# Kernel optimization log

Hardware: AMD Instinct MI355X
Metric: run time of the kernel (lower is better)

The kernel has to match this reference:

```python
import jax, jax.numpy as jnp
import numpy as np

C = 1.0      # base manifold curvature (Lorentz c)
C_E = 1.0    # expert manifold curvature (all experts init to c=1.0)
K = 1        # n_activated_experts (top-k)
SCALE = 2.0  # LResNet scale for shared-expert combine
EPS = 1e-8


def _lorentz_swiglu(x, W1, W3, W2, c_mid, c_out, prescale):
    """LorentzExpert / LorentzFeedForward: SwiGLU on space coords with Lorentz time lift.
    x: [T, D] (full Lorentz vector). W1,W3: [I-1, D]; W2: [D-1, I]. Returns [T, D]."""
    if prescale:
        x = x * np.float32(np.sqrt(C_E / C))  # x * sqrt(c_expert / c)
    s1 = jax.nn.silu(x @ W1.T)                 # [T, I-1] w1(x, return_space=True)
    s3 = x @ W3.T                              # [T, I-1] w3(x, return_space=True)
    sp = s1 * s3                               # gated space part
    t = jnp.sqrt(jnp.clip((sp * sp).sum(-1, keepdims=True) + c_mid, EPS))
    h = jnp.concatenate([t, sp], axis=-1)      # [T, I] point on expert manifold
    o = h @ W2.T                               # [T, D-1] w2 space output
    ot = jnp.sqrt(jnp.clip((o * o).sum(-1, keepdims=True) + c_out, EPS))
    return jnp.concatenate([ot, o], axis=-1)   # [T, D] on base manifold


def setup_inputs() -> dict:
    key = jax.random.key(0)
    ks = jax.random.split(key, 9)
    T, D, E, I = 2048, 1024, 8, 1024
    x = jax.random.normal(ks[0], (T, D), jnp.float32)
    gate_w = jax.random.normal(ks[1], (E, D - 1), jnp.float32) / np.sqrt(D - 1)
    gate_b = jax.random.normal(ks[2], (E,), jnp.float32) * 0.01
    W1 = jax.random.normal(ks[3], (E, I - 1, D), jnp.float32) / np.sqrt(D)
    W3 = jax.random.normal(ks[4], (E, I - 1, D), jnp.float32) / np.sqrt(D)
    W2 = jax.random.normal(ks[5], (E, D - 1, I), jnp.float32) / np.sqrt(I)
    Ws1 = jax.random.normal(ks[6], (I - 1, D), jnp.float32) / np.sqrt(D)
    Ws3 = jax.random.normal(ks[7], (I - 1, D), jnp.float32) / np.sqrt(D)
    Ws2 = jax.random.normal(ks[8], (D - 1, I), jnp.float32) / np.sqrt(I)
    return {"x": x, "gate_w": gate_w, "gate_b": gate_b, "W1": W1, "W3": W3,
            "W2": W2, "Ws1": Ws1, "Ws3": Ws3, "Ws2": Ws2}


def reference(x, gate_w, gate_b, W1, W3, W2, Ws1, Ws3, Ws2):
    T, D = x.shape
    E = gate_w.shape[0]
    # ---- Gate (softmax scoring, n_groups == 1, route_scale == 1.0) ----
    logits = x[:, 1:] @ gate_w.T                                    # [T, E]
    scores = jax.nn.softmax(logits.astype(jnp.float32), axis=-1)
    biased = scores + gate_b                                        # bias only affects routing
    _, idx = jax.lax.top_k(biased, K)                               # [T, K]
    weights = jnp.take_along_axis(scores, idx, axis=-1).astype(x.dtype)  # [T, K]
    # dense per-token expert gate weights [T, E]
    oh = jax.nn.one_hot(idx, E, dtype=x.dtype)                      # [T, K, E]
    gw = (oh * weights[..., None]).sum(axis=1)                      # [T, E]
    # ---- y init: project(zeros) -> [sqrt(c), 0, ..., 0] ----
    y0 = jnp.concatenate([jnp.full((T, 1), np.sqrt(C), x.dtype),
                          jnp.zeros((T, D - 1), x.dtype)], axis=-1)
    # ---- routed experts (dense reference: every expert on every token, masked combine) ----
    e_out = jax.vmap(lambda w1, w3, w2: _lorentz_swiglu(x, w1, w3, w2, C_E, C, True))(W1, W3, W2)  # [E, T, D]
    y = y0 + jnp.einsum('te,etd->td', gw, e_out)
    # ---- shared expert (LorentzFeedForward, stays on base manifold) ----
    z = _lorentz_swiglu(x, Ws1, Ws3, Ws2, C, C, False)
    # ---- LResNet weighted sum: normalize (z + scale*y) back to manifold ----
    comb = z + SCALE * y
    li = (comb[:, 1:] ** 2).sum(-1, keepdims=True) - comb[:, :1] ** 2  # Lorentz inner <comb,comb>
    out = np.float32(np.sqrt(C)) * comb / jnp.sqrt(jnp.clip(jnp.abs(li), EPS))
    return out
```

## Files before the change

### kernel.cpp

```cpp
#include <hip/hip_runtime.h>

typedef __bf16 bf16;
typedef __attribute__((ext_vector_type(8))) __bf16 bf16x8;
typedef __attribute__((ext_vector_type(4))) float floatx4;

#define TOK 2048
#define DD  1024
#define NE  8
#define SMAX 24

#define MFMA16(A,B,C) __builtin_amdgcn_mfma_f32_16x16x32_bf16(A,B,C,0,0,0)

__device__ __forceinline__ void load_lds16(const bf16* g, bf16* l) {
  __builtin_amdgcn_global_load_lds(
      (const __attribute__((address_space(1))) void*)g,
      (__attribute__((address_space(3))) void*)l, 16, 0, 0);
}

#define WBAR(N) asm volatile("s_waitcnt vmcnt(" #N ")\n\ts_barrier" ::: "memory")
#define BARO    asm volatile("s_barrier" ::: "memory")

#define NCVT (8*2046 + 2046 + 8*1023 + 1023)
#define GATEB TOK
#define ZEROB TOK
__global__ __launch_bounds__(256) void prep_kernel(
    const float* __restrict__ x, const float* __restrict__ gate_w,
    const float* __restrict__ gate_b,
    const float* __restrict__ W1, const float* __restrict__ W3,
    const float* __restrict__ W2, const float* __restrict__ Ws1,
    const float* __restrict__ Ws3, const float* __restrict__ Ws2,
    bf16* __restrict__ x_bf, int* __restrict__ eidx, float* __restrict__ ewgt,
    float* __restrict__ ss,
    bf16* __restrict__ w13, bf16* __restrict__ ws13,
    bf16* __restrict__ w2b, bf16* __restrict__ ws2b,
    float* __restrict__ o_r, float* __restrict__ o_s)
{
  const int bid = blockIdx.x, tid = threadIdx.x;

  if (bid >= GATEB) {
    if (bid >= GATEB + NCVT) {
      const int t = bid - (GATEB + NCVT);
      const float4 z = {0.f, 0.f, 0.f, 0.f};
      ((float4*)(o_r + (size_t)t * 1024))[tid] = z;
      ((float4*)(o_s + (size_t)t * 1024))[tid] = z;
      return;
    }
    const int r = bid - GATEB;
    const float* src; bf16* dst;
    if (r < 8 * 2046) {
      const int e = r / 2046, q = r % 2046;
      src = ((q & 1) ? W3 : W1) + ((size_t)e * 1023 + (q >> 1)) * 1024;
      dst = w13 + (size_t)r * 1024;
    } else if (r < 8 * 2046 + 2046) {
      const int q = r - 8 * 2046;
      src = ((q & 1) ? Ws3 : Ws1) + (size_t)(q >> 1) * 1024;
      dst = ws13 + (size_t)q * 1024;
    } else if (r < 8 * 2046 + 2046 + 8 * 1023) {
      const int q = r - (8 * 2046 + 2046);
      src = W2 + (size_t)q * 1024;
      dst = w2b + (size_t)q * 1024;
    } else {
      const int q = r - (8 * 2046 + 2046 + 8 * 1023);
      src = Ws2 + (size_t)q * 1024;
      dst = ws2b + (size_t)q * 1024;
    }
    const float4 f = ((const float4*)src)[tid];
    union { bf16 h[4]; uint2 u; } p;
    p.h[0] = (bf16)f.x; p.h[1] = (bf16)f.y; p.h[2] = (bf16)f.z; p.h[3] = (bf16)f.w;
    ((uint2*)dst)[tid] = p.u;
    return;
  }

  const int t = bid;
  if (tid < 2) ss[tid * TOK + t] = 0.f;
  const float4 v = ((const float4*)(x + (size_t)t * DD))[tid];
  union { bf16 h[4]; uint2 u; } pk;
  pk.h[0] = (bf16)v.x; pk.h[1] = (bf16)v.y; pk.h[2] = (bf16)v.z; pk.h[3] = (bf16)v.w;
  ((uint2*)(x_bf + (size_t)t * DD))[tid] = pk.u;

  float acc[NE];
#pragma unroll
  for (int e = 0; e < NE; ++e) acc[e] = 0.f;
  const float vv[4] = {v.x, v.y, v.z, v.w};
#pragma unroll
  for (int i = 0; i < 4; ++i) {
    const int d = tid * 4 + i;
    if (d >= 1) {
#pragma unroll
      for (int e = 0; e < NE; ++e) acc[e] += vv[i] * gate_w[e * (DD - 1) + d - 1];
    }
  }
#pragma unroll
  for (int off = 32; off > 0; off >>= 1) {
#pragma unroll
    for (int e = 0; e < NE; ++e) acc[e] += __shfl_down(acc[e], off);
  }
  __shared__ float red[4][NE];
  const int wid = tid >> 6, lane = tid & 63;
  if (lane == 0) {
#pragma unroll
    for (int e = 0; e < NE; ++e) red[wid][e] = acc[e];
  }
  __syncthreads();
  if (tid == 0) {
    float lg[NE];
#pragma unroll
    for (int e = 0; e < NE; ++e) lg[e] = red[0][e] + red[1][e] + red[2][e] + red[3][e];
    float m = lg[0];
    for (int e = 1; e < NE; ++e) m = fmaxf(m, lg[e]);
    float ex[NE], s = 0.f;
    for (int e = 0; e < NE; ++e) { ex[e] = expf(lg[e] - m); s += ex[e]; }
    const float inv = 1.f / s;
    int best = 0; float bb = ex[0] * inv + gate_b[0];
    for (int e = 1; e < NE; ++e) {
      const float b = ex[e] * inv + gate_b[e];
      if (b > bb) { bb = b; best = e; }
    }
    eidx[t] = best;
    ewgt[t] = ex[best] * inv;
  }
}

__global__ __launch_bounds__(256) void route_kernel(
    const int* __restrict__ eidx, int* __restrict__ perm,
    int* __restrict__ pos_of, int4* __restrict__ wl, int* __restrict__ n1)
{
  __shared__ int cnt[NE], off[NE], bas[NE + 1];
  const int tid = threadIdx.x;
  if (tid < NE) cnt[tid] = 0;
  __syncthreads();
  for (int t = tid; t < TOK; t += 256) atomicAdd(&cnt[eidx[t]], 1);
  __syncthreads();
  if (tid == 0) {
    int run = 0;
    for (int e = 0; e < NE; ++e) { bas[e] = run; off[e] = run; run += cnt[e]; }
    bas[NE] = run;
    int n = 0;
    for (int e = 0; e < NE; ++e)
      for (int r0 = 0; r0 < cnt[e]; r0 += 256) {
        int rows = cnt[e] - r0; if (rows > 256) rows = 256;
        wl[n++] = make_int4(bas[e] + r0, rows, e, 0);
      }
    for (int r0 = 0; r0 < TOK; r0 += 256) wl[n++] = make_int4(r0, 256, NE, 0);
    *n1 = n;
  }
  __syncthreads();
  for (int t = tid; t < TOK; t += 256) {
    const int e = eidx[t];
    const int p = atomicAdd(&off[e], 1);
    perm[p] = t;
    pos_of[t] = p;
  }
}

__global__ __launch_bounds__(1024) void mlp1_kernel(
    const bf16* __restrict__ x_bf, const bf16* __restrict__ w13,
    const bf16* __restrict__ ws13,
    const int* __restrict__ perm, const int4* __restrict__ wl,
    const int* __restrict__ wl_n,
    bf16* __restrict__ h_r, bf16* __restrict__ h_s,
    float* __restrict__ ss_r, float* __restrict__ ss_z)
{
  const int bid = blockIdx.x;
  const int slot = bid % SMAX, nt = bid / SMAX;
  if (slot >= *wl_n) return;
  const int4 wle = wl[slot];
  const int mbase = wle.x, rows = wle.y, eid = wle.z;
  const int tid = threadIdx.x;
  const bool routed = (eid < NE);
  const bf16* bmat = routed ? w13 + (size_t)eid * 2046 * 1024 : ws13;
  bf16* hbuf  = routed ? h_r : h_s;
  float* ssbuf = routed ? ss_r : ss_z;

  extern __shared__ __align__(16) bf16 smem[];
  bf16* const Asb[2] = {smem, smem + 16384};
  bf16* const Bsb[2] = {smem + 32768, smem + 49152};
  __shared__ int toks[256];
  if (tid < 256) {
    int r = tid < rows ? tid : rows - 1;
    toks[tid] = routed ? perm[mbase + r] : (mbase + r);
  }
  __syncthreads();

  const int wid = tid >> 6, lane = tid & 63;
  const int srow = lane >> 3;
  const int kbg  = (lane & 7) ^ (srow & 7);
  const bf16 *aG0, *aG1, *bG0, *bG1;
  int aL0o, aL1o, bL0o, bL1o;
  {
    const int r0 = wid * 16;
    aG0 = x_bf + (size_t)toks[r0 + 0 + srow] * 1024 + kbg * 8;
    aG1 = x_bf + (size_t)toks[r0 + 8 + srow] * 1024 + kbg * 8;
    aL0o = (r0 + 0) * 64; aL1o = (r0 + 8) * 64;
    int b0 = nt * 256 + r0 + 0 + srow; if (b0 > 2045) b0 = 2045;
    int b1 = nt * 256 + r0 + 8 + srow; if (b1 > 2045) b1 = 2045;
    bG0 = bmat + (size_t)b0 * 1024 + kbg * 8;
    bG1 = bmat + (size_t)b1 * 1024 + kbg * 8;
    bL0o = (r0 + 0) * 64; bL1o = (r0 + 8) * 64;
  }

  const int lrow = lane & 15, quad = lane >> 4, sw = lane & 7;
  const int wrow = (wid >> 2) * 64, wcol = (wid & 3) * 64;
  int aoff[4], boff[4], koff[2];
#pragma unroll
  for (int mi = 0; mi < 4; ++mi) aoff[mi] = (wrow + mi * 16 + lrow) * 64;
#pragma unroll
  for (int ni = 0; ni < 4; ++ni) boff[ni] = (wcol + ni * 16 + lrow) * 64;
#pragma unroll
  for (int kk = 0; kk < 2; ++kk) koff[kk] = ((kk * 4 + quad) ^ sw) * 8;

  const floatx4 fz = {0.f, 0.f, 0.f, 0.f};
  floatx4 acc[4][4];
#pragma unroll
  for (int mi = 0; mi < 4; ++mi)
#pragma unroll
    for (int ni = 0; ni < 4; ++ni) acc[mi][ni] = fz;

#define STAGE1(KE, BUF) { \
    load_lds16(aG0 + (KE), Asb[BUF] + aL0o); load_lds16(aG1 + (KE), Asb[BUF] + aL1o); \
    load_lds16(bG0 + (KE), Bsb[BUF] + bL0o); load_lds16(bG1 + (KE), Bsb[BUF] + bL1o); }

#define COMP1(BUF) { \
_Pragma("unroll") \
    for (int kk = 0; kk < 2; ++kk) { \
      bf16x8 av[4], bv[4]; \
_Pragma("unroll") \
      for (int mi = 0; mi < 4; ++mi) av[mi] = *(const bf16x8*)(Asb[BUF] + aoff[mi] + koff[kk]); \
_Pragma("unroll") \
      for (int ni = 0; ni < 4; ++ni) bv[ni] = *(const bf16x8*)(Bsb[BUF] + boff[ni] + koff[kk]); \
_Pragma("unroll") \
      for (int mi = 0; mi < 4; ++mi) \
_Pragma("unroll") \
        for (int ni = 0; ni < 4; ++ni) \
          acc[mi][ni] = MFMA16(av[mi], bv[ni], acc[mi][ni]); \
    } }

  STAGE1(0, 0)
  STAGE1(64, 1)
#pragma unroll 1
  for (int t = 0; t < 7; ++t) {
    const int ke = t * 128;
    WBAR(4); COMP1(0) BARO; STAGE1(ke + 128, 0)
    WBAR(4); COMP1(1) BARO; STAGE1(ke + 192, 1)
  }
  WBAR(4); COMP1(0)
  WBAR(0); COMP1(1)
#undef STAGE1
#undef COMP1

#pragma unroll
  for (int mi = 0; mi < 4; ++mi) {
#pragma unroll
    for (int r = 0; r < 4; ++r) {
      const int row = wrow + mi * 16 + quad * 4 + r;
      const bool rowok = row < rows;
      float ssum = 0.f;
#pragma unroll
      for (int ni = 0; ni < 4; ++ni) {
        const float c = acc[mi][ni][r];
        const float partner = __shfl_xor(c, 1);
        const float s1 = (lane & 1) ? partner : c;
        const float s3 = (lane & 1) ? c : partner;
        const float sp = (s1 / (1.f + __expf(-s1))) * s3;
        const int P = (nt * 256 + wcol + ni * 16 + lrow) >> 1;
        const bool ok = rowok && ((lane & 1) == 0) && (P < 1023);
        if (ok) hbuf[(size_t)(mbase + row) * 1024 + 1 + P] = (bf16)sp;
        ssum += ok ? sp * sp : 0.f;
      }
      ssum += __shfl_xor(ssum, 1);
      ssum += __shfl_xor(ssum, 2);
      ssum += __shfl_xor(ssum, 4);
      ssum += __shfl_xor(ssum, 8);
      if (lrow == 0 && rowok) atomicAdd(ssbuf + mbase + row, ssum);
    }
  }
}

__global__ __launch_bounds__(256) void finalize_t_kernel(
    const float* __restrict__ ss_r, const float* __restrict__ ss_z,
    bf16* __restrict__ h_r, bf16* __restrict__ h_s)
{
  const int i = blockIdx.x * 256 + threadIdx.x;
  if (i < TOK) {
    h_r[(size_t)i * 1024] = (bf16)sqrtf(ss_r[i] + 1.0f);
    h_s[(size_t)i * 1024] = (bf16)sqrtf(ss_z[i] + 1.0f);
  }
}

__global__ __launch_bounds__(1024) void mlp2_kernel(
    const bf16* __restrict__ h_r, const bf16* __restrict__ h_s,
    const bf16* __restrict__ w2b, const bf16* __restrict__ ws2b,
    const int4* __restrict__ wl, const int* __restrict__ wl_n,
    float* __restrict__ o_r, float* __restrict__ o_s)
{
  const int bid = blockIdx.x;
  const int slot = bid % SMAX;
  const int rest = bid / SMAX;
  const int nt = rest & 3, kh = rest >> 2;
  if (slot >= *wl_n) return;
  const int4 wle = wl[slot];
  const int mbase = wle.x, rows = wle.y, eid = wle.z;
  const int tid = threadIdx.x;
  const bool routed = (eid < NE);
  const bf16* abuf = routed ? h_r : h_s;
  const bf16* bmat = routed ? w2b + (size_t)eid * 1023 * 1024 : ws2b;
  float* obuf = routed ? o_r : o_s;
  const int n0 = nt * 256;
  const int kbase = kh * 512;

  extern __shared__ __align__(16) bf16 smem[];
  bf16* const Asb[2] = {smem, smem + 16384};
  bf16* const Bsb[2] = {smem + 32768, smem + 49152};

  const int wid = tid >> 6, lane = tid & 63;
  const int srow = lane >> 3;
  const int kbg  = (lane & 7) ^ (srow & 7);
  const bf16 *aG0, *aG1, *bG0, *bG1;
  int aL0o, aL1o, bL0o, bL1o;
  {
    const int r0 = wid * 16;
    int ra0 = r0 + 0 + srow; if (ra0 >= rows) ra0 = rows - 1;
    int ra1 = r0 + 8 + srow; if (ra1 >= rows) ra1 = rows - 1;
    aG0 = abuf + (size_t)(mbase + ra0) * 1024 + kbase + kbg * 8;
    aG1 = abuf + (size_t)(mbase + ra1) * 1024 + kbase + kbg * 8;
    aL0o = (r0 + 0) * 64; aL1o = (r0 + 8) * 64;
    int b0 = n0 + r0 + 0 + srow; if (b0 > 1022) b0 = 1022;
    int b1 = n0 + r0 + 8 + srow; if (b1 > 1022) b1 = 1022;
    bG0 = bmat + (size_t)b0 * 1024 + kbase + kbg * 8;
    bG1 = bmat + (size_t)b1 * 1024 + kbase + kbg * 8;
    bL0o = (r0 + 0) * 64; bL1o = (r0 + 8) * 64;
  }

  const int lrow = lane & 15, quad = lane >> 4, sw = lane & 7;
  const int wrow = (wid >> 2) * 64, wcol = (wid & 3) * 64;
  int aoff[4], boff[4], koff[2];
#pragma unroll
  for (int mi = 0; mi < 4; ++mi) aoff[mi] = (wrow + mi * 16 + lrow) * 64;
#pragma unroll
  for (int ni = 0; ni < 4; ++ni) boff[ni] = (wcol + ni * 16 + lrow) * 64;
#pragma unroll
  for (int kk = 0; kk < 2; ++kk) koff[kk] = ((kk * 4 + quad) ^ sw) * 8;

  const floatx4 fz = {0.f, 0.f, 0.f, 0.f};
  floatx4 acc[4][4];
#pragma unroll
  for (int mi = 0; mi < 4; ++mi)
#pragma unroll
    for (int ni = 0; ni < 4; ++ni) acc[mi][ni] = fz;

#define STAGE2(KE, BUF) { \
    load_lds16(aG0 + (KE), Asb[BUF] + aL0o); load_lds16(aG1 + (KE), Asb[BUF] + aL1o); \
    load_lds16(bG0 + (KE), Bsb[BUF] + bL0o); load_lds16(bG1 + (KE), Bsb[BUF] + bL1o); }

#define COMP2(BUF) { \
_Pragma("unroll") \
    for (int kk = 0; kk < 2; ++kk) { \
      bf16x8 av[4], bv[4]; \
_Pragma("unroll") \
      for (int mi = 0; mi < 4; ++mi) av[mi] = *(const bf16x8*)(Asb[BUF] + aoff[mi] + koff[kk]); \
_Pragma("unroll") \
      for (int ni = 0; ni < 4; ++ni) bv[ni] = *(const bf16x8*)(Bsb[BUF] + boff[ni] + koff[kk]); \
_Pragma("unroll") \
      for (int mi = 0; mi < 4; ++mi) \
_Pragma("unroll") \
        for (int ni = 0; ni < 4; ++ni) \
          acc[mi][ni] = MFMA16(av[mi], bv[ni], acc[mi][ni]); \
    } }

  STAGE2(0, 0)
  STAGE2(64, 1)
#pragma unroll 1
  for (int t = 0; t < 3; ++t) {
    const int ke = t * 128;
    WBAR(4); COMP2(0) BARO; STAGE2(ke + 128, 0)
    WBAR(4); COMP2(1) BARO; STAGE2(ke + 192, 1)
  }
  WBAR(4); COMP2(0)
  WBAR(0); COMP2(1)
#undef STAGE2
#undef COMP2

#pragma unroll
  for (int mi = 0; mi < 4; ++mi) {
#pragma unroll
    for (int r = 0; r < 4; ++r) {
      const int row = wrow + mi * 16 + quad * 4 + r;
      if (row < rows) {
        float* orow = obuf + (size_t)(mbase + row) * 1024;
#pragma unroll
        for (int ni = 0; ni < 4; ++ni) {
          const int n = n0 + wcol + ni * 16 + lrow;
          if (n < 1023) atomicAdd(orow + n, acc[mi][ni][r]);
        }
      }
    }
  }
}

__global__ __launch_bounds__(256) void combine_kernel(
    const float* __restrict__ o_r, const float* __restrict__ o_s,
    const int* __restrict__ pos_of, const float* __restrict__ wgt,
    float* __restrict__ out)
{
  const int t = blockIdx.x, tid = threadIdx.x;
  const int p = pos_of[t];
  const float w = wgt[t];
  const float4 oz = ((const float4*)(o_s + (size_t)t * 1024))[tid];
  const float4 oe = ((const float4*)(o_r + (size_t)p * 1024))[tid];
  const float tw = 2.f * w;
  float c0 = oz.x + tw * oe.x;
  float c1 = oz.y + tw * oe.y;
  float c2 = oz.z + tw * oe.z;
  float c3 = (tid == 255) ? 0.f : (oz.w + tw * oe.w);
  float sc = c0 * c0 + c1 * c1 + c2 * c2 + c3 * c3;
  float sz = oz.x * oz.x + oz.y * oz.y + oz.z * oz.z + ((tid == 255) ? 0.f : oz.w * oz.w);
  float sr = oe.x * oe.x + oe.y * oe.y + oe.z * oe.z + ((tid == 255) ? 0.f : oe.w * oe.w);
#pragma unroll
  for (int off = 32; off > 0; off >>= 1) {
    sc += __shfl_down(sc, off);
    sz += __shfl_down(sz, off);
    sr += __shfl_down(sr, off);
  }
  __shared__ float rs[3][4];
  if ((tid & 63) == 0) {
    rs[0][tid >> 6] = sc; rs[1][tid >> 6] = sz; rs[2][tid >> 6] = sr;
  }
  __syncthreads();
  const float space2 = rs[0][0] + rs[0][1] + rs[0][2] + rs[0][3];
  const float ss_oz  = rs[1][0] + rs[1][1] + rs[1][2] + rs[1][3];
  const float ss_or  = rs[2][0] + rs[2][1] + rs[2][2] + rs[2][3];
  const float comb0 = sqrtf(ss_oz + 1.f) + 2.f + 2.f * w * sqrtf(ss_or + 1.f);
  const float li = space2 - comb0 * comb0;
  const float inv = 1.f / sqrtf(fmaxf(fabsf(li), 1e-8f));
  float* orow = out + (size_t)t * 1024;
  const int j = 1 + tid * 4;
  orow[j]     = c0 * inv;
  orow[j + 1] = c1 * inv;
  orow[j + 2] = c2 * inv;
  if (tid != 255) orow[j + 3] = c3 * inv;
  if (tid == 0) orow[0] = comb0 * inv;
}

extern "C" void kernel_launch(void* const* d_in, const int* in_sizes, int n_in,
                              void* d_out, int out_size, void* d_ws, size_t ws_size,
                              hipStream_t stream) {
  const float* x      = (const float*)d_in[0];
  const float* gate_w = (const float*)d_in[1];
  const float* gate_b = (const float*)d_in[2];
  const float* W1     = (const float*)d_in[3];
  const float* W3     = (const float*)d_in[4];
  const float* W2     = (const float*)d_in[5];
  const float* Ws1    = (const float*)d_in[6];
  const float* Ws3    = (const float*)d_in[7];
  const float* Ws2    = (const float*)d_in[8];
  float* out = (float*)d_out;

  char* ws = (char*)d_ws;
  size_t off = 0;
  auto alloc = [&](size_t bytes) {
    void* p = ws + off;
    off += (bytes + 255) & ~(size_t)255;
    return p;
  };
  bf16*  x_bf = (bf16*) alloc((size_t)TOK * 1024 * 2);
  bf16*  h_r  = (bf16*) alloc((size_t)TOK * 1024 * 2);
  bf16*  h_s  = (bf16*) alloc((size_t)TOK * 1024 * 2);
  float* o_r  = (float*)alloc((size_t)TOK * 1024 * 4);
  float* o_s  = (float*)alloc((size_t)TOK * 1024 * 4);
  float* ss   = (float*)alloc((size_t)2 * TOK * 4);
  int*   eidx = (int*)  alloc((size_t)TOK * 4);
  float* ewgt = (float*)alloc((size_t)TOK * 4);
  int*   perm = (int*)  alloc((size_t)TOK * 4);
  int*   posf = (int*)  alloc((size_t)TOK * 4);
  int4*  wl1  = (int4*) alloc((size_t)SMAX * 16);
  int*   wn   = (int*)  alloc(32);
  bf16*  w13  = (bf16*) alloc((size_t)8 * 2046 * 1024 * 2);
  bf16*  ws13 = (bf16*) alloc((size_t)2046 * 1024 * 2);
  bf16*  w2b  = (bf16*) alloc((size_t)8 * 1023 * 1024 * 2);
  bf16*  ws2b = (bf16*) alloc((size_t)1023 * 1024 * 2);

  float* ss_r  = ss;
  float* ss_z  = ss + TOK;

  const int MLP_LDS = 2 * (256 * 64 + 256 * 64) * 2;
  (void)hipFuncSetAttribute((const void*)mlp1_kernel,
                            hipFuncAttributeMaxDynamicSharedMemorySize, MLP_LDS);
  (void)hipFuncSetAttribute((const void*)mlp2_kernel,
                            hipFuncAttributeMaxDynamicSharedMemorySize, MLP_LDS);

  prep_kernel<<<GATEB + NCVT + ZEROB, 256, 0, stream>>>(
      x, gate_w, gate_b, W1, W3, W2, Ws1, Ws3, Ws2,
      x_bf, eidx, ewgt, ss, w13, ws13, w2b, ws2b, o_r, o_s);
  route_kernel<<<1, 256, 0, stream>>>(eidx, perm, posf, wl1, wn);
  mlp1_kernel<<<8 * SMAX, 1024, MLP_LDS, stream>>>(x_bf, w13, ws13, perm, wl1, wn,
                                                   h_r, h_s, ss_r, ss_z);
  finalize_t_kernel<<<8, 256, 0, stream>>>(ss_r, ss_z, h_r, h_s);
  mlp2_kernel<<<8 * SMAX, 1024, MLP_LDS, stream>>>(h_r, h_s, w2b, ws2b, wl1, wn,
                                                   o_r, o_s);
  combine_kernel<<<TOK, 256, 0, stream>>>(o_r, o_s, posf, ewgt, out);
}
```

Before: 248.1 us.

## Replace mlp2 atomics with split-K partial buffers and fold time column into combine

The second-layer GEMM now writes its two K-halves with plain stores into separate buffers instead of doing atomicAdd into zero-initialised outputs. This removes the zeroing blocks in prep and the finalize_t kernel. The h time coordinate is set to zero during prep, and its contribution (t times the first column of W2, kept in fp32) is added back in combine, along with the sum of the two partials. The second partial buffers reuse the w13 weight workspace, which is dead by then. Combine must now read two extra rows per token.

```diff
diff --git a/kernel.cpp b/kernel.cpp
--- a/kernel.cpp
+++ b/kernel.cpp
@@ -22,7 +22,6 @@
 
 #define NCVT (8*2046 + 2046 + 8*1023 + 1023)
 #define GATEB TOK
-#define ZEROB TOK
 __global__ __launch_bounds__(256) void prep_kernel(
     const float* __restrict__ x, const float* __restrict__ gate_w,
     const float* __restrict__ gate_b,
@@ -33,20 +32,15 @@
     float* __restrict__ ss,
     bf16* __restrict__ w13, bf16* __restrict__ ws13,
     bf16* __restrict__ w2b, bf16* __restrict__ ws2b,
-    float* __restrict__ o_r, float* __restrict__ o_s)
+    float* __restrict__ w2c0_r, float* __restrict__ w2c0_s,
+    bf16* __restrict__ h_r, bf16* __restrict__ h_s)
 {
   const int bid = blockIdx.x, tid = threadIdx.x;
 
   if (bid >= GATEB) {
-    if (bid >= GATEB + NCVT) {
-      const int t = bid - (GATEB + NCVT);
-      const float4 z = {0.f, 0.f, 0.f, 0.f};
-      ((float4*)(o_r + (size_t)t * 1024))[tid] = z;
-      ((float4*)(o_s + (size_t)t * 1024))[tid] = z;
-      return;
-    }
     const int r = bid - GATEB;
     const float* src; bf16* dst;
+    float* c0dst = nullptr;
     if (r < 8 * 2046) {
       const int e = r / 2046, q = r % 2046;
       src = ((q & 1) ? W3 : W1) + ((size_t)e * 1023 + (q >> 1)) * 1024;
@@ -59,12 +53,15 @@
       const int q = r - (8 * 2046 + 2046);
       src = W2 + (size_t)q * 1024;
       dst = w2b + (size_t)q * 1024;
+      c0dst = w2c0_r + (size_t)(q / 1023) * 1024 + (q % 1023);
     } else {
       const int q = r - (8 * 2046 + 2046 + 8 * 1023);
       src = Ws2 + (size_t)q * 1024;
       dst = ws2b + (size_t)q * 1024;
+      c0dst = w2c0_s + q;
     }
     const float4 f = ((const float4*)src)[tid];
+    if (tid == 0 && c0dst) *c0dst = f.x;
     union { bf16 h[4]; uint2 u; } p;
     p.h[0] = (bf16)f.x; p.h[1] = (bf16)f.y; p.h[2] = (bf16)f.z; p.h[3] = (bf16)f.w;
     ((uint2*)dst)[tid] = p.u;
@@ -73,6 +70,8 @@
 
   const int t = bid;
   if (tid < 2) ss[tid * TOK + t] = 0.f;
+  if (tid == 2) h_r[(size_t)t * 1024] = (bf16)0.f;
+  if (tid == 3) h_s[(size_t)t * 1024] = (bf16)0.f;
   const float4 v = ((const float4*)(x + (size_t)t * DD))[tid];
   union { bf16 h[4]; uint2 u; } pk;
   pk.h[0] = (bf16)v.x; pk.h[1] = (bf16)v.y; pk.h[2] = (bf16)v.z; pk.h[3] = (bf16)v.w;
@@ -276,22 +275,12 @@
   }
 }
 
-__global__ __launch_bounds__(256) void finalize_t_kernel(
-    const float* __restrict__ ss_r, const float* __restrict__ ss_z,
-    bf16* __restrict__ h_r, bf16* __restrict__ h_s)
-{
-  const int i = blockIdx.x * 256 + threadIdx.x;
-  if (i < TOK) {
-    h_r[(size_t)i * 1024] = (bf16)sqrtf(ss_r[i] + 1.0f);
-    h_s[(size_t)i * 1024] = (bf16)sqrtf(ss_z[i] + 1.0f);
-  }
-}
-
 __global__ __launch_bounds__(1024) void mlp2_kernel(
     const bf16* __restrict__ h_r, const bf16* __restrict__ h_s,
     const bf16* __restrict__ w2b, const bf16* __restrict__ ws2b,
     const int4* __restrict__ wl, const int* __restrict__ wl_n,
-    float* __restrict__ o_r, float* __restrict__ o_s)
+    float* __restrict__ o_r0, float* __restrict__ o_r1,
+    float* __restrict__ o_s0, float* __restrict__ o_s1)
 {
   const int bid = blockIdx.x;
   const int slot = bid % SMAX;
@@ -304,7 +293,7 @@
   const bool routed = (eid < NE);
   const bf16* abuf = routed ? h_r : h_s;
   const bf16* bmat = routed ? w2b + (size_t)eid * 1023 * 1024 : ws2b;
-  float* obuf = routed ? o_r : o_s;
+  float* obuf = routed ? (kh ? o_r1 : o_r0) : (kh ? o_s1 : o_s0);
   const int n0 = nt * 256;
   const int kbase = kh * 512;
 
@@ -390,7 +379,7 @@
 #pragma unroll
         for (int ni = 0; ni < 4; ++ni) {
           const int n = n0 + wcol + ni * 16 + lrow;
-          if (n < 1023) atomicAdd(orow + n, acc[mi][ni][r]);
+          if (n < 1023) orow[n] = acc[mi][ni][r];
         }
       }
     }
@@ -398,23 +387,42 @@
 }
 
 __global__ __launch_bounds__(256) void combine_kernel(
-    const float* __restrict__ o_r, const float* __restrict__ o_s,
-    const int* __restrict__ pos_of, const float* __restrict__ wgt,
-    float* __restrict__ out)
+    const float* __restrict__ o_r0, const float* __restrict__ o_r1,
+    const float* __restrict__ o_s0, const float* __restrict__ o_s1,
+    const float* __restrict__ ss_r, const float* __restrict__ ss_z,
+    const float* __restrict__ w2c0_r, const float* __restrict__ w2c0_s,
+    const int* __restrict__ eidx, const int* __restrict__ pos_of,
+    const float* __restrict__ wgt, float* __restrict__ out)
 {
   const int t = blockIdx.x, tid = threadIdx.x;
   const int p = pos_of[t];
+  const int e = eidx[t];
   const float w = wgt[t];
-  const float4 oz = ((const float4*)(o_s + (size_t)t * 1024))[tid];
-  const float4 oe = ((const float4*)(o_r + (size_t)p * 1024))[tid];
+  const float tz = sqrtf(ss_z[t] + 1.f);
+  const float tr = sqrtf(ss_r[p] + 1.f);
+  const float4 oz0 = ((const float4*)(o_s0 + (size_t)t * 1024))[tid];
+  const float4 oz1 = ((const float4*)(o_s1 + (size_t)t * 1024))[tid];
+  const float4 oe0 = ((const float4*)(o_r0 + (size_t)p * 1024))[tid];
+  const float4 oe1 = ((const float4*)(o_r1 + (size_t)p * 1024))[tid];
+  const float4 c0s = ((const float4*)(w2c0_s))[tid];
+  const float4 c0r = ((const float4*)(w2c0_r + (size_t)e * 1024))[tid];
+  const bool last = (tid == 255);
+  float ozf0 = oz0.x + oz1.x + tz * c0s.x;
+  float ozf1 = oz0.y + oz1.y + tz * c0s.y;
+  float ozf2 = oz0.z + oz1.z + tz * c0s.z;
+  float ozf3 = last ? 0.f : (oz0.w + oz1.w + tz * c0s.w);
+  float oef0 = oe0.x + oe1.x + tr * c0r.x;
+  float oef1 = oe0.y + oe1.y + tr * c0r.y;
+  float oef2 = oe0.z + oe1.z + tr * c0r.z;
+  float oef3 = last ? 0.f : (oe0.w + oe1.w + tr * c0r.w);
   const float tw = 2.f * w;
-  float c0 = oz.x + tw * oe.x;
-  float c1 = oz.y + tw * oe.y;
-  float c2 = oz.z + tw * oe.z;
-  float c3 = (tid == 255) ? 0.f : (oz.w + tw * oe.w);
+  const float c0 = ozf0 + tw * oef0;
+  const float c1 = ozf1 + tw * oef1;
+  const float c2 = ozf2 + tw * oef2;
+  const float c3 = ozf3 + tw * oef3;
   float sc = c0 * c0 + c1 * c1 + c2 * c2 + c3 * c3;
-  float sz = oz.x * oz.x + oz.y * oz.y + oz.z * oz.z + ((tid == 255) ? 0.f : oz.w * oz.w);
-  float sr = oe.x * oe.x + oe.y * oe.y + oe.z * oe.z + ((tid == 255) ? 0.f : oe.w * oe.w);
+  float sz = ozf0 * ozf0 + ozf1 * ozf1 + ozf2 * ozf2 + ozf3 * ozf3;
+  float sr = oef0 * oef0 + oef1 * oef1 + oef2 * oef2 + oef3 * oef3;
 #pragma unroll
   for (int off = 32; off > 0; off >>= 1) {
     sc += __shfl_down(sc, off);
@@ -437,7 +445,7 @@
   orow[j]     = c0 * inv;
   orow[j + 1] = c1 * inv;
   orow[j + 2] = c2 * inv;
-  if (tid != 255) orow[j + 3] = c3 * inv;
+  if (!last) orow[j + 3] = c3 * inv;
   if (tid == 0) orow[0] = comb0 * inv;
 }
 
@@ -465,8 +473,8 @@
   bf16*  x_bf = (bf16*) alloc((size_t)TOK * 1024 * 2);
   bf16*  h_r  = (bf16*) alloc((size_t)TOK * 1024 * 2);
   bf16*  h_s  = (bf16*) alloc((size_t)TOK * 1024 * 2);
-  float* o_r  = (float*)alloc((size_t)TOK * 1024 * 4);
-  float* o_s  = (float*)alloc((size_t)TOK * 1024 * 4);
+  float* o_r0 = (float*)alloc((size_t)TOK * 1024 * 4);
+  float* o_s0 = (float*)alloc((size_t)TOK * 1024 * 4);
   float* ss   = (float*)alloc((size_t)2 * TOK * 4);
   int*   eidx = (int*)  alloc((size_t)TOK * 4);
   float* ewgt = (float*)alloc((size_t)TOK * 4);
@@ -474,10 +482,15 @@
   int*   posf = (int*)  alloc((size_t)TOK * 4);
   int4*  wl1  = (int4*) alloc((size_t)SMAX * 16);
   int*   wn   = (int*)  alloc(32);
+  float* w2c0_r = (float*)alloc((size_t)NE * 1024 * 4);
+  float* w2c0_s = (float*)alloc((size_t)1024 * 4);
   bf16*  w13  = (bf16*) alloc((size_t)8 * 2046 * 1024 * 2);
   bf16*  ws13 = (bf16*) alloc((size_t)2046 * 1024 * 2);
   bf16*  w2b  = (bf16*) alloc((size_t)8 * 1023 * 1024 * 2);
   bf16*  ws2b = (bf16*) alloc((size_t)1023 * 1024 * 2);
+
+  float* o_r1 = (float*)w13;
+  float* o_s1 = (float*)w13 + (size_t)TOK * 1024;
 
   float* ss_r  = ss;
   float* ss_z  = ss + TOK;
@@ -488,14 +501,14 @@
   (void)hipFuncSetAttribute((const void*)mlp2_kernel,
                             hipFuncAttributeMaxDynamicSharedMemorySize, MLP_LDS);
 
-  prep_kernel<<<GATEB + NCVT + ZEROB, 256, 0, stream>>>(
+  prep_kernel<<<GATEB + NCVT, 256, 0, stream>>>(
       x, gate_w, gate_b, W1, W3, W2, Ws1, Ws3, Ws2,
-      x_bf, eidx, ewgt, ss, w13, ws13, w2b, ws2b, o_r, o_s);
+      x_bf, eidx, ewgt, ss, w13, ws13, w2b, ws2b, w2c0_r, w2c0_s, h_r, h_s);
   route_kernel<<<1, 256, 0, stream>>>(eidx, perm, posf, wl1, wn);
   mlp1_kernel<<<8 * SMAX, 1024, MLP_LDS, stream>>>(x_bf, w13, ws13, perm, wl1, wn,
                                                    h_r, h_s, ss_r, ss_z);
-  finalize_t_kernel<<<8, 256, 0, stream>>>(ss_r, ss_z, h_r, h_s);
   mlp2_kernel<<<8 * SMAX, 1024, MLP_LDS, stream>>>(h_r, h_s, w2b, ws2b, wl1, wn,
-                                                   o_r, o_s);
-  combine_kernel<<<TOK, 256, 0, stream>>>(o_r, o_s, posf, ewgt, out);
-}
+                                                   o_r0, o_r1, o_s0, o_s1);
+  combine_kernel<<<TOK, 256, 0, stream>>>(o_r0, o_r1, o_s0, o_s1, ss_r, ss_z,
+                                          w2c0_r, w2c0_s, eidx, posf, ewgt, out);
+}
```

Measured after the change: 231.6 us. -6.7%, faster.
